# Kernel tuning notes

Hardware: AMD Instinct MI355X
Metric: run time of the kernel (lower is better)

The kernel has to match this reference:

```python
import jax, jax.numpy as jnp
import numpy as np

DIM = 1024
HEADS = 16
DIM_HEAD = 64
INNER = HEADS * DIM_HEAD  # 1024


def setup_inputs() -> dict:
    key = jax.random.key(0)
    ks = jax.random.split(key, 5)
    B, N = 4, 2048
    x = jax.random.normal(ks[0], (B, N, DIM), dtype=jnp.float32)
    # nn.Linear weights stored as [out, in]; we keep [in, out] for x @ W
    s = 1.0 / np.sqrt(DIM)
    Wq = jax.random.uniform(ks[1], (DIM, INNER), jnp.float32, -s, s)
    Wkv = jax.random.uniform(ks[2], (DIM, 2 * INNER), jnp.float32, -s, s)
    so = 1.0 / np.sqrt(INNER)
    Wo = jax.random.uniform(ks[3], (INNER, DIM), jnp.float32, -so, so)
    bo = jax.random.uniform(ks[4], (DIM,), jnp.float32, -so, so)
    return {"x": x, "Wq": Wq, "Wkv": Wkv, "Wo": Wo, "bo": bo}


def reference(x, Wq, Wkv, Wo, bo):
    B, N, _ = x.shape
    scale = DIM_HEAD ** -0.5
    q = x @ Wq                      # [B, N, INNER]
    kv = x @ Wkv                    # [B, N, 2*INNER]
    k, v = jnp.split(kv, 2, axis=-1)

    def split_heads(t):
        return t.reshape(B, N, HEADS, DIM_HEAD).transpose(0, 2, 1, 3)  # b h n d

    q, k, v = map(split_heads, (q, k, v))
    dots = jnp.einsum('bhid,bhjd->bhij', q, k) * scale
    # causal mask: positions j > i filled with -inf
    causal = jnp.triu(jnp.ones((N, N), dtype=bool), k=1)
    dots = jnp.where(causal, -jnp.inf, dots)
    attn = jax.nn.softmax(dots, axis=-1)
    out = jnp.einsum('bhij,bhjd->bhid', attn, v)
    out = out.transpose(0, 2, 1, 3).reshape(B, N, INNER)
    return out @ Wo + bo
```

## Files before the change

### kernel.cpp

```cpp
#include <hip/hip_runtime.h>
#include <hip/hip_bf16.h>
#include <math.h>

typedef __attribute__((ext_vector_type(8))) short bf16x8;
typedef __attribute__((ext_vector_type(4))) float f32x4;

static __device__ inline ushort f2bf(float f) {
    union { float f; unsigned u; } v; v.f = f;
    unsigned r = (v.u + 0x7fff + ((v.u >> 16) & 1)) >> 16;
    return (ushort)r;
}

#define GLD_LDS(g, l) \
    __builtin_amdgcn_global_load_lds( \
        (const __attribute__((address_space(1))) void*)(g), \
        (__attribute__((address_space(3))) void*)(l), 16, 0, 0)

__global__ __launch_bounds__(256) void convert_x(
    const float* __restrict__ x, ushort* __restrict__ xb)
{
    const size_t i = ((size_t)blockIdx.x * 256 + threadIdx.x) * 8;
    float4 a = *(const float4*)(x + i);
    float4 b = *(const float4*)(x + i + 4);
    bf16x8 t;
    t[0] = (short)f2bf(a.x); t[1] = (short)f2bf(a.y);
    t[2] = (short)f2bf(a.z); t[3] = (short)f2bf(a.w);
    t[4] = (short)f2bf(b.x); t[5] = (short)f2bf(b.y);
    t[6] = (short)f2bf(b.z); t[7] = (short)f2bf(b.w);
    *(bf16x8*)(xb + i) = t;
}

__global__ __launch_bounds__(256) void prep_w(
    const float* __restrict__ Wq, const float* __restrict__ Wkv,
    const float* __restrict__ Wo, ushort* __restrict__ Wt)
{
    const int w = threadIdx.x >> 6;
    const int lane = threadIdx.x & 63;
    const int tile = blockIdx.x * 4 + w;
    const int r0 = (tile >> 4) << 6;
    const int k0 = (tile & 15) << 6;

    const float* src; int ld, c0;
    if (r0 < 1024)      { src = Wq;  ld = 1024; c0 = r0; }
    else if (r0 < 3072) { src = Wkv; ld = 2048; c0 = r0 - 1024; }
    else                { src = Wo;  ld = 1024; c0 = r0 - 3072; }

    ushort v[64];
    #pragma unroll
    for (int k = 0; k < 64; ++k)
        v[k] = f2bf(src[(size_t)(k0 + k) * ld + c0 + lane]);

    ushort* dst = Wt + (size_t)(r0 + lane) * 1024 + k0;
    #pragma unroll
    for (int k = 0; k < 64; k += 8) {
        bf16x8 t;
        #pragma unroll
        for (int j = 0; j < 8; ++j) t[j] = (short)v[k + j];
        *(bf16x8*)(dst + k) = t;
    }
}

#define GEMM_MAIN_LOOP(Aptr, Btptr)                                            \
    __shared__ ushort As[128 * 32];                                            \
    __shared__ ushort Bs[128 * 32];                                            \
    const int tid = threadIdx.x;                                               \
    const int lane = tid & 63;                                                 \
    const int w = tid >> 6;                                                    \
    const int l15 = lane & 15;                                                 \
    const int quad = lane >> 4;                                                \
    const int wm = w & 1, wn = w >> 1;                                         \
    const int rowBase = blockIdx.y * 128;                                      \
    const int colBase = blockIdx.x * 128;                                      \
    const int sRow = lane >> 2;                                                \
    const int sOff = (lane & 3) * 8;                                           \
    const ushort* aG0 = (Aptr) + (size_t)(rowBase + (w*2+0)*16 + sRow) * 1024 + sOff; \
    const ushort* aG1 = (Aptr) + (size_t)(rowBase + (w*2+1)*16 + sRow) * 1024 + sOff; \
    const ushort* bG0 = (Btptr) + (size_t)(colBase + (w*2+0)*16 + sRow) * 1024 + sOff; \
    const ushort* bG1 = (Btptr) + (size_t)(colBase + (w*2+1)*16 + sRow) * 1024 + sOff; \
    ushort* aL0 = As + (w*2+0)*512;                                            \
    ushort* aL1 = As + (w*2+1)*512;                                            \
    ushort* bL0 = Bs + (w*2+0)*512;                                            \
    ushort* bL1 = Bs + (w*2+1)*512;                                            \
    f32x4 acc[4][4];                                                           \
    _Pragma("unroll")                                                          \
    for (int i = 0; i < 4; ++i)                                                \
        _Pragma("unroll")                                                      \
        for (int j = 0; j < 4; ++j) acc[i][j] = (f32x4){0.f,0.f,0.f,0.f};      \
    for (int k0 = 0; k0 < 1024; k0 += 32) {                                    \
        __syncthreads();                                                       \
        GLD_LDS(aG0 + k0, aL0);                                                \
        GLD_LDS(aG1 + k0, aL1);                                                \
        GLD_LDS(bG0 + k0, bL0);                                                \
        GLD_LDS(bG1 + k0, bL1);                                                \
        __syncthreads();                                                       \
        bf16x8 af[4], bf[4];                                                   \
        _Pragma("unroll")                                                      \
        for (int mi = 0; mi < 4; ++mi)                                         \
            af[mi] = *(const bf16x8*)&As[(wm*64 + mi*16 + l15)*32 + quad*8];   \
        _Pragma("unroll")                                                      \
        for (int ni = 0; ni < 4; ++ni)                                         \
            bf[ni] = *(const bf16x8*)&Bs[(wn*64 + ni*16 + l15)*32 + quad*8];   \
        _Pragma("unroll")                                                      \
        for (int mi = 0; mi < 4; ++mi)                                         \
            _Pragma("unroll")                                                  \
            for (int ni = 0; ni < 4; ++ni)                                     \
                acc[mi][ni] = __builtin_amdgcn_mfma_f32_16x16x32_bf16(         \
                    af[mi], bf[ni], acc[mi][ni], 0, 0, 0);                     \
    }

__global__ __launch_bounds__(256) void gemm_qkv(
    const ushort* __restrict__ A, const ushort* __restrict__ Bt,
    ushort* __restrict__ Qb, ushort* __restrict__ Kb, ushort* __restrict__ Vt)
{
    GEMM_MAIN_LOOP(A, Bt)

    const int seg = colBase >> 10;
    if (seg == 2) {
        #pragma unroll
        for (int mi = 0; mi < 4; ++mi) {
            #pragma unroll
            for (int ni = 0; ni < 4; ++ni) {
                const int c = (colBase + wn*64 + ni*16 + l15) & 1023;
                const int h = c >> 6, d = c & 63;
                const int m = rowBase + wm*64 + mi*16 + quad*4;
                const int b = m >> 11, nn = m & 2047;
                ushort4 v;
                v.x = f2bf(acc[mi][ni][0]); v.y = f2bf(acc[mi][ni][1]);
                v.z = f2bf(acc[mi][ni][2]); v.w = f2bf(acc[mi][ni][3]);
                *(ushort4*)(Vt + ((size_t)(b*16 + h)*64 + d)*2048 + nn) = v;
            }
        }
    } else {
        ushort* dst = seg ? Kb : Qb;
        const float sc = seg ? 1.0f : 0.18033688011112042f;
        #pragma unroll
        for (int mi = 0; mi < 4; ++mi) {
            #pragma unroll
            for (int ni = 0; ni < 4; ++ni) {
                const int c = (colBase + wn*64 + ni*16 + l15) & 1023;
                const int h = c >> 6, d = c & 63;
                #pragma unroll
                for (int r = 0; r < 4; ++r) {
                    const int m = rowBase + wm*64 + mi*16 + quad*4 + r;
                    const int b = m >> 11, nn = m & 2047;
                    dst[((((size_t)b*16 + h)*2048 + nn) << 6) + d] = f2bf(acc[mi][ni][r] * sc);
                }
            }
        }
    }
}

__global__ __launch_bounds__(256) void gemm_out(
    const ushort* __restrict__ A, const ushort* __restrict__ Bt,
    const float* __restrict__ bo, float* __restrict__ out)
{
    GEMM_MAIN_LOOP(A, Bt)

    #pragma unroll
    for (int mi = 0; mi < 4; ++mi) {
        #pragma unroll
        for (int ni = 0; ni < 4; ++ni) {
            const int n = colBase + wn*64 + ni*16 + l15;
            const float bb = bo[n];
            #pragma unroll
            for (int r = 0; r < 4; ++r) {
                const int m = rowBase + wm*64 + mi*16 + quad*4 + r;
                out[(size_t)m * 1024 + n] = acc[mi][ni][r] + bb;
            }
        }
    }
}

__device__ __forceinline__ bf16x8 lds_frag(const ushort* S, int row, int chunk) {
    return *(const bf16x8*)(S + row * 64 + ((chunk ^ (row & 7)) << 3));
}

__global__ __launch_bounds__(256, 2) void flash_mfma(
    const ushort* __restrict__ Qb,
    const ushort* __restrict__ Kb,
    const ushort* __restrict__ Vt,
    ushort* __restrict__ Ob)
{
    __shared__ ushort Ks[2][4096];
    __shared__ ushort Vs[2][4096];
    __shared__ ushort PsAll[4][32][72];

    const int tid = threadIdx.x;
    const int w = tid >> 6;
    const int lane = tid & 63;
    const int l15 = lane & 15;
    const int quad = lane >> 4;
    ushort (*Ps)[72] = PsAll[w];

    const int blk = blockIdx.x;
    const int bh = ((blk & 7) << 3) | ((blk >> 3) & 7);
    const int p = blk >> 6;
    const int qtHi = 15 - p, qtLo = p;
    const int ntHi = 2 * qtHi + 2;
    const int total = 34;

    const int rb[2] = { (qtHi << 7) + w * 32, (qtLo << 7) + w * 32 };

    const int sr0 = tid >> 3, sr1 = sr0 + 32;
    const int cg0 = (tid & 7) ^ (sr0 & 7);
    const int cg1 = (tid & 7) ^ (sr1 & 7);
    const ushort* kgb = Kb + (size_t)bh * 131072;
    const ushort* vgb = Vt + (size_t)bh * 131072;

    bf16x8 qf[2][2][2];
    #pragma unroll
    for (int p_ = 0; p_ < 2; ++p_)
        #pragma unroll
        for (int mi = 0; mi < 2; ++mi) {
            const ushort* qp = Qb + ((size_t)bh * 2048 + rb[p_] + mi*16 + l15) * 64 + quad * 8;
            qf[p_][mi][0] = *(const bf16x8*)qp;
            qf[p_][mi][1] = *(const bf16x8*)(qp + 32);
        }

    bf16x8 bones;
    #pragma unroll
    for (int j = 0; j < 8; ++j) bones[j] = (short)0x3F80;

    float m_r[2][2];
    f32x4 o[2][2][4], lacc[2][2];
    #pragma unroll
    for (int p_ = 0; p_ < 2; ++p_)
        #pragma unroll
        for (int mi = 0; mi < 2; ++mi) {
            m_r[p_][mi] = -INFINITY;
            lacc[p_][mi] = (f32x4){0.f, 0.f, 0.f, 0.f};
            #pragma unroll
            for (int nb = 0; nb < 4; ++nb) o[p_][mi][nb] = (f32x4){0.f, 0.f, 0.f, 0.f};
        }

    GLD_LDS(kgb + 0*4096 + sr0*64 + cg0*8, &Ks[0][tid*8]);
    GLD_LDS(kgb + 0*4096 + sr1*64 + cg1*8, &Ks[0][tid*8 + 2048]);
    GLD_LDS(vgb + (size_t)sr0*2048 + 0*64 + cg0*8, &Vs[0][tid*8]);
    GLD_LDS(vgb + (size_t)sr1*2048 + 0*64 + cg1*8, &Vs[0][tid*8 + 2048]);

    for (int t = 0; t < total; ++t) {
        __syncthreads();
        const int cur = t & 1;
        if (t + 1 < total) {
            const int tn = t + 1;
            const int jn = (tn < ntHi) ? tn : tn - ntHi;
            ushort* kd = &Ks[cur ^ 1][tid * 8];
            ushort* vd = &Vs[cur ^ 1][tid * 8];
            GLD_LDS(kgb + (size_t)jn*4096 + sr0*64 + cg0*8, kd);
            GLD_LDS(kgb + (size_t)jn*4096 + sr1*64 + cg1*8, kd + 2048);
            GLD_LDS(vgb + (size_t)sr0*2048 + jn*64 + cg0*8, vd);
            GLD_LDS(vgb + (size_t)sr1*2048 + jn*64 + cg1*8, vd + 2048);
        }
        const int p_ = (t >= ntHi);
        const int jt = p_ ? t - ntHi : t;
        const int j0 = jt << 6;
        const int rb0 = rb[p_];
        if (j0 > rb0 + 31) continue;

        const ushort* Ksb = Ks[cur];
        const ushort* Vsb = Vs[cur];

        f32x4 St[2][4];
        #pragma unroll
        for (int kb = 0; kb < 4; ++kb) {
            bf16x8 ka = lds_frag(Ksb, kb*16 + l15, quad);
            bf16x8 kc = lds_frag(Ksb, kb*16 + l15, quad + 4);
            #pragma unroll
            for (int mi = 0; mi < 2; ++mi) {
                f32x4 s = (f32x4){0.f, 0.f, 0.f, 0.f};
                s = __builtin_amdgcn_mfma_f32_16x16x32_bf16(ka, qf[p_][mi][0], s, 0, 0, 0);
                s = __builtin_amdgcn_mfma_f32_16x16x32_bf16(kc, qf[p_][mi][1], s, 0, 0, 0);
                St[mi][kb] = s;
            }
        }

        #pragma unroll
        for (int mi = 0; mi < 2; ++mi) {
            const int qrow = rb0 + mi*16 + l15;
            if (j0 + 63 > rb0 + mi*16) {
                #pragma unroll
                for (int kb = 0; kb < 4; ++kb) {
                    const int kbase = j0 + kb*16 + quad*4;
                    #pragma unroll
                    for (int r = 0; r < 4; ++r)
                        if (kbase + r > qrow) St[mi][kb][r] = -INFINITY;
                }
            }
            f32x4 mv = St[mi][0];
            #pragma unroll
            for (int kb = 1; kb < 4; ++kb)
                #pragma unroll
                for (int r = 0; r < 4; ++r) mv[r] = fmaxf(mv[r], St[mi][kb][r]);
            float mx = fmaxf(fmaxf(mv[0], mv[1]), fmaxf(mv[2], mv[3]));
            mx = fmaxf(mx, __shfl_xor(mx, 16));
            mx = fmaxf(mx, __shfl_xor(mx, 32));
            const float mold = m_r[p_][mi];
            const float mnew = fmaxf(mold, mx);
            m_r[p_][mi] = mnew;
            const float corr = __builtin_amdgcn_exp2f(mold - mnew);
            #pragma unroll
            for (int kb = 0; kb < 4; ++kb)
                #pragma unroll
                for (int r = 0; r < 4; ++r)
                    St[mi][kb][r] = __builtin_amdgcn_exp2f(St[mi][kb][r] - mnew);
            #pragma unroll
            for (int kb = 0; kb < 4; ++kb) {
                union { float f; unsigned u; } c0, c1, c2, c3;
                c0.f = St[mi][kb][0]; c1.f = St[mi][kb][1];
                c2.f = St[mi][kb][2]; c3.f = St[mi][kb][3];
                uint2 pk;
                pk.x = (c0.u >> 16) | (c1.u & 0xFFFF0000u);
                pk.y = (c2.u >> 16) | (c3.u & 0xFFFF0000u);
                *(uint2*)&Ps[mi*16 + l15][kb*16 + quad*4] = pk;
            }
            float ct[4];
            #pragma unroll
            for (int r = 0; r < 4; ++r) ct[r] = __shfl(corr, quad*4 + r);
            #pragma unroll
            for (int r = 0; r < 4; ++r) lacc[p_][mi][r] *= ct[r];
            #pragma unroll
            for (int nb = 0; nb < 4; ++nb)
                #pragma unroll
                for (int r = 0; r < 4; ++r) o[p_][mi][nb][r] *= ct[r];
        }

        bf16x8 pf[2][2];
        #pragma unroll
        for (int mi = 0; mi < 2; ++mi) {
            pf[mi][0] = *(const bf16x8*)&Ps[mi*16 + l15][quad * 8];
            pf[mi][1] = *(const bf16x8*)&Ps[mi*16 + l15][32 + quad * 8];
        }
        #pragma unroll
        for (int mi = 0; mi < 2; ++mi) {
            lacc[p_][mi] = __builtin_amdgcn_mfma_f32_16x16x32_bf16(pf[mi][0], bones, lacc[p_][mi], 0, 0, 0);
            lacc[p_][mi] = __builtin_amdgcn_mfma_f32_16x16x32_bf16(pf[mi][1], bones, lacc[p_][mi], 0, 0, 0);
        }
        #pragma unroll
        for (int nb = 0; nb < 4; ++nb) {
            bf16x8 va = lds_frag(Vsb, nb*16 + l15, quad);
            bf16x8 vc = lds_frag(Vsb, nb*16 + l15, quad + 4);
            #pragma unroll
            for (int mi = 0; mi < 2; ++mi) {
                o[p_][mi][nb] = __builtin_amdgcn_mfma_f32_16x16x32_bf16(pf[mi][0], va, o[p_][mi][nb], 0, 0, 0);
                o[p_][mi][nb] = __builtin_amdgcn_mfma_f32_16x16x32_bf16(pf[mi][1], vc, o[p_][mi][nb], 0, 0, 0);
            }
        }
    }

    const int b = bh >> 4, h = bh & 15;
    #pragma unroll
    for (int p_ = 0; p_ < 2; ++p_)
        #pragma unroll
        for (int mi = 0; mi < 2; ++mi)
            #pragma unroll
            for (int r = 0; r < 4; ++r) {
                const int ig = rb[p_] + mi*16 + quad*4 + r;
                const float inv = 1.f / lacc[p_][mi][r];
                ushort* op = Ob + ((size_t)(b * 2048 + ig)) * 1024 + h * 64 + l15;
                #pragma unroll
                for (int nb = 0; nb < 4; ++nb)
                    op[nb * 16] = f2bf(o[p_][mi][nb][r] * inv);
            }
}

extern "C" void kernel_launch(void* const* d_in, const int* in_sizes, int n_in,
                              void* d_out, int out_size, void* d_ws, size_t ws_size,
                              hipStream_t stream) {
    const float* x   = (const float*)d_in[0];
    const float* Wq  = (const float*)d_in[1];
    const float* Wkv = (const float*)d_in[2];
    const float* Wo  = (const float*)d_in[3];
    const float* bo  = (const float*)d_in[4];
    float* out = (float*)d_out;

    const size_t SEG = (size_t)8388608 * 2;
    char* ws = (char*)d_ws;
    ushort* xb = (ushort*)(ws);
    ushort* Qb = (ushort*)(ws + SEG);
    ushort* Kb = (ushort*)(ws + SEG * 2);
    ushort* Vt = (ushort*)(ws + SEG * 3);
    ushort* Ob = (ushort*)(ws + SEG * 4);
    ushort* Wt = (ushort*)(ws + SEG * 5);

    convert_x<<<dim3(4096), 256, 0, stream>>>(x, xb);
    prep_w<<<dim3(256), 256, 0, stream>>>(Wq, Wkv, Wo, Wt);
    gemm_qkv<<<dim3(24, 64), 256, 0, stream>>>(xb, Wt, Qb, Kb, Vt);
    flash_mfma<<<dim3(512), 256, 0, stream>>>(Qb, Kb, Vt, Ob);
    gemm_out<<<dim3(8, 64), 256, 0, stream>>>(Ob, Wt + (size_t)3072 * 1024, bo, out);
}
```

Measured before the change: 296.6 us.

## Split paired causal query tiles into separate blocks and skip no-op rescales

The flash attention kernel no longer pairs a heavy and a light causal query tile in one block. It now launches 1024 blocks, each handling a single 128-row query tile, ordered heaviest first, which halves the per-thread accumulator and Q-fragment state. The online-softmax rescale of the output and row-sum accumulators is also skipped when no lane's running max increased. This trades the static per-block load balance for more blocks, less register pressure and possibly higher occupancy, relying on the scheduler to balance the uneven tile costs.

```diff
diff --git a/kernel.cpp b/kernel.cpp
--- a/kernel.cpp
+++ b/kernel.cpp
@@ -194,12 +194,9 @@
 
     const int blk = blockIdx.x;
     const int bh = ((blk & 7) << 3) | ((blk >> 3) & 7);
-    const int p = blk >> 6;
-    const int qtHi = 15 - p, qtLo = p;
-    const int ntHi = 2 * qtHi + 2;
-    const int total = 34;
-
-    const int rb[2] = { (qtHi << 7) + w * 32, (qtLo << 7) + w * 32 };
+    const int qt = 15 - (blk >> 6);
+    const int nt = 2 * qt + 2;
+    const int rb0 = (qt << 7) + w * 32;
 
     const int sr0 = tid >> 3, sr1 = sr0 + 32;
     const int cg0 = (tid & 7) ^ (sr0 & 7);
@@ -207,43 +204,38 @@
     const ushort* kgb = Kb + (size_t)bh * 131072;
     const ushort* vgb = Vt + (size_t)bh * 131072;
 
-    bf16x8 qf[2][2][2];
-    #pragma unroll
-    for (int p_ = 0; p_ < 2; ++p_)
-        #pragma unroll
-        for (int mi = 0; mi < 2; ++mi) {
-            const ushort* qp = Qb + ((size_t)bh * 2048 + rb[p_] + mi*16 + l15) * 64 + quad * 8;
-            qf[p_][mi][0] = *(const bf16x8*)qp;
-            qf[p_][mi][1] = *(const bf16x8*)(qp + 32);
-        }
+    bf16x8 qf[2][2];
+    #pragma unroll
+    for (int mi = 0; mi < 2; ++mi) {
+        const ushort* qp = Qb + ((size_t)bh * 2048 + rb0 + mi*16 + l15) * 64 + quad * 8;
+        qf[mi][0] = *(const bf16x8*)qp;
+        qf[mi][1] = *(const bf16x8*)(qp + 32);
+    }
 
     bf16x8 bones;
     #pragma unroll
     for (int j = 0; j < 8; ++j) bones[j] = (short)0x3F80;
 
-    float m_r[2][2];
-    f32x4 o[2][2][4], lacc[2][2];
-    #pragma unroll
-    for (int p_ = 0; p_ < 2; ++p_)
-        #pragma unroll
-        for (int mi = 0; mi < 2; ++mi) {
-            m_r[p_][mi] = -INFINITY;
-            lacc[p_][mi] = (f32x4){0.f, 0.f, 0.f, 0.f};
-            #pragma unroll
-            for (int nb = 0; nb < 4; ++nb) o[p_][mi][nb] = (f32x4){0.f, 0.f, 0.f, 0.f};
-        }
-
-    GLD_LDS(kgb + 0*4096 + sr0*64 + cg0*8, &Ks[0][tid*8]);
-    GLD_LDS(kgb + 0*4096 + sr1*64 + cg1*8, &Ks[0][tid*8 + 2048]);
-    GLD_LDS(vgb + (size_t)sr0*2048 + 0*64 + cg0*8, &Vs[0][tid*8]);
-    GLD_LDS(vgb + (size_t)sr1*2048 + 0*64 + cg1*8, &Vs[0][tid*8 + 2048]);
-
-    for (int t = 0; t < total; ++t) {
+    float m_r[2];
+    f32x4 o[2][4], lacc[2];
+    #pragma unroll
+    for (int mi = 0; mi < 2; ++mi) {
+        m_r[mi] = -INFINITY;
+        lacc[mi] = (f32x4){0.f, 0.f, 0.f, 0.f};
+        #pragma unroll
+        for (int nb = 0; nb < 4; ++nb) o[mi][nb] = (f32x4){0.f, 0.f, 0.f, 0.f};
+    }
+
+    GLD_LDS(kgb + sr0*64 + cg0*8, &Ks[0][tid*8]);
+    GLD_LDS(kgb + sr1*64 + cg1*8, &Ks[0][tid*8 + 2048]);
+    GLD_LDS(vgb + (size_t)sr0*2048 + cg0*8, &Vs[0][tid*8]);
+    GLD_LDS(vgb + (size_t)sr1*2048 + cg1*8, &Vs[0][tid*8 + 2048]);
+
+    for (int t = 0; t < nt; ++t) {
         __syncthreads();
         const int cur = t & 1;
-        if (t + 1 < total) {
-            const int tn = t + 1;
-            const int jn = (tn < ntHi) ? tn : tn - ntHi;
+        if (t + 1 < nt) {
+            const int jn = t + 1;
             ushort* kd = &Ks[cur ^ 1][tid * 8];
             ushort* vd = &Vs[cur ^ 1][tid * 8];
             GLD_LDS(kgb + (size_t)jn*4096 + sr0*64 + cg0*8, kd);
@@ -251,10 +243,7 @@
             GLD_LDS(vgb + (size_t)sr0*2048 + jn*64 + cg0*8, vd);
             GLD_LDS(vgb + (size_t)sr1*2048 + jn*64 + cg1*8, vd + 2048);
         }
-        const int p_ = (t >= ntHi);
-        const int jt = p_ ? t - ntHi : t;
-        const int j0 = jt << 6;
-        const int rb0 = rb[p_];
+        const int j0 = t << 6;
         if (j0 > rb0 + 31) continue;
 
         const ushort* Ksb = Ks[cur];
@@ -268,8 +257,8 @@
             #pragma unroll
             for (int mi = 0; mi < 2; ++mi) {
                 f32x4 s = (f32x4){0.f, 0.f, 0.f, 0.f};
-                s = __builtin_amdgcn_mfma_f32_16x16x32_bf16(ka, qf[p_][mi][0], s, 0, 0, 0);
-                s = __builtin_amdgcn_mfma_f32_16x16x32_bf16(kc, qf[p_][mi][1], s, 0, 0, 0);
+                s = __builtin_amdgcn_mfma_f32_16x16x32_bf16(ka, qf[mi][0], s, 0, 0, 0);
+                s = __builtin_amdgcn_mfma_f32_16x16x32_bf16(kc, qf[mi][1], s, 0, 0, 0);
                 St[mi][kb] = s;
             }
         }
@@ -294,10 +283,21 @@
             float mx = fmaxf(fmaxf(mv[0], mv[1]), fmaxf(mv[2], mv[3]));
             mx = fmaxf(mx, __shfl_xor(mx, 16));
             mx = fmaxf(mx, __shfl_xor(mx, 32));
-            const float mold = m_r[p_][mi];
+            const float mold = m_r[mi];
             const float mnew = fmaxf(mold, mx);
-            m_r[p_][mi] = mnew;
-            const float corr = __builtin_amdgcn_exp2f(mold - mnew);
+            if (__any(mnew > mold)) {
+                m_r[mi] = mnew;
+                const float corr = __builtin_amdgcn_exp2f(mold - mnew);
+                float ct[4];
+                #pragma unroll
+                for (int r = 0; r < 4; ++r) ct[r] = __shfl(corr, quad*4 + r);
+                #pragma unroll
+                for (int r = 0; r < 4; ++r) lacc[mi][r] *= ct[r];
+                #pragma unroll
+                for (int nb = 0; nb < 4; ++nb)
+                    #pragma unroll
+                    for (int r = 0; r < 4; ++r) o[mi][nb][r] *= ct[r];
+            }
             #pragma unroll
             for (int kb = 0; kb < 4; ++kb)
                 #pragma unroll
@@ -313,15 +313,6 @@
                 pk.y = (c2.u >> 16) | (c3.u & 0xFFFF0000u);
                 *(uint2*)&Ps[mi*16 + l15][kb*16 + quad*4] = pk;
             }
-            float ct[4];
-            #pragma unroll
-            for (int r = 0; r < 4; ++r) ct[r] = __shfl(corr, quad*4 + r);
-            #pragma unroll
-            for (int r = 0; r < 4; ++r) lacc[p_][mi][r] *= ct[r];
-            #pragma unroll
-            for (int nb = 0; nb < 4; ++nb)
-                #pragma unroll
-                for (int r = 0; r < 4; ++r) o[p_][mi][nb][r] *= ct[r];
         }
 
         bf16x8 pf[2][2];
@@ -332,8 +323,8 @@
         }
         #pragma unroll
         for (int mi = 0; mi < 2; ++mi) {
-            lacc[p_][mi] = __builtin_amdgcn_mfma_f32_16x16x32_bf16(pf[mi][0], bones, lacc[p_][mi], 0, 0, 0);
-            lacc[p_][mi] = __builtin_amdgcn_mfma_f32_16x16x32_bf16(pf[mi][1], bones, lacc[p_][mi], 0, 0, 0);
+            lacc[mi] = __builtin_amdgcn_mfma_f32_16x16x32_bf16(pf[mi][0], bones, lacc[mi], 0, 0, 0);
+            lacc[mi] = __builtin_amdgcn_mfma_f32_16x16x32_bf16(pf[mi][1], bones, lacc[mi], 0, 0, 0);
         }
         #pragma unroll
         for (int nb = 0; nb < 4; ++nb) {
@@ -341,26 +332,24 @@
             bf16x8 vc = lds_frag(Vsb, nb*16 + l15, quad + 4);
             #pragma unroll
             for (int mi = 0; mi < 2; ++mi) {
-                o[p_][mi][nb] = __builtin_amdgcn_mfma_f32_16x16x32_bf16(pf[mi][0], va, o[p_][mi][nb], 0, 0, 0);
-                o[p_][mi][nb] = __builtin_amdgcn_mfma_f32_16x16x32_bf16(pf[mi][1], vc, o[p_][mi][nb], 0, 0, 0);
+                o[mi][nb] = __builtin_amdgcn_mfma_f32_16x16x32_bf16(pf[mi][0], va, o[mi][nb], 0, 0, 0);
+                o[mi][nb] = __builtin_amdgcn_mfma_f32_16x16x32_bf16(pf[mi][1], vc, o[mi][nb], 0, 0, 0);
             }
         }
     }
 
     const int b = bh >> 4, h = bh & 15;
     #pragma unroll
-    for (int p_ = 0; p_ < 2; ++p_)
-        #pragma unroll
-        for (int mi = 0; mi < 2; ++mi)
-            #pragma unroll
-            for (int r = 0; r < 4; ++r) {
-                const int ig = rb[p_] + mi*16 + quad*4 + r;
-                const float inv = 1.f / lacc[p_][mi][r];
-                ushort* op = Ob + ((size_t)(b * 2048 + ig)) * 1024 + h * 64 + l15;
-                #pragma unroll
-                for (int nb = 0; nb < 4; ++nb)
-                    op[nb * 16] = f2bf(o[p_][mi][nb][r] * inv);
-            }
+    for (int mi = 0; mi < 2; ++mi)
+        #pragma unroll
+        for (int r = 0; r < 4; ++r) {
+            const int ig = rb0 + mi*16 + quad*4 + r;
+            const float inv = 1.f / lacc[mi][r];
+            ushort* op = Ob + ((size_t)(b * 2048 + ig)) * 1024 + h * 64 + l15;
+            #pragma unroll
+            for (int nb = 0; nb < 4; ++nb)
+                op[nb * 16] = f2bf(o[mi][nb][r] * inv);
+        }
 }
 
 extern "C" void kernel_launch(void* const* d_in, const int* in_sizes, int n_in,
@@ -385,6 +374,6 @@
     convert_x<<<dim3(4096), 256, 0, stream>>>(x, xb);
     prep_w<<<dim3(256), 256, 0, stream>>>(Wq, Wkv, Wo, Wt);
     gemm_qkv<<<dim3(24, 64), 256, 0, stream>>>(xb, Wt, Qb, Kb, Vt);
-    flash_mfma<<<dim3(512), 256, 0, stream>>>(Qb, Kb, Vt, Ob);
+    flash_mfma<<<dim3(1024), 256, 0, stream>>>(Qb, Kb, Vt, Ob);
     gemm_out<<<dim3(8, 64), 256, 0, stream>>>(Ob, Wt + (size_t)3072 * 1024, bo, out);
 }
```

Result: faster. 259.6 us (-12.5%).
